# Optimization experiments

Measured on AMD Instinct MI355X. Metric: run time of the kernel, lower is better.

The kernel has to match this reference:

```python
import jax, jax.numpy as jnp
import numpy as np

B, T, D, U = 32, 2048, 512, 512


def setup_inputs() -> dict:
    key = jax.random.key(0)
    ks = jax.random.split(key, 6)
    value = jax.random.normal(ks[0], (B, T, D), dtype=jnp.float32)
    query = jax.random.normal(ks[1], (B, D), dtype=jnp.float32)
    mask = jax.random.randint(ks[2], (B, T), 0, 2, dtype=jnp.int32)
    # Glorot-ish scaled dense weights (no bias, matching Dense(use_bias=False))
    W1 = jax.random.normal(ks[3], (D, U), dtype=jnp.float32) * (1.0 / np.sqrt(D))
    W2 = jax.random.normal(ks[4], (D, U), dtype=jnp.float32) * (1.0 / np.sqrt(D))
    V = jax.random.normal(ks[5], (U,), dtype=jnp.float32) * (1.0 / np.sqrt(U))
    return {"value": value, "query": query, "mask": mask, "W1": W1, "W2": W2, "V": V}


def reference(value, query, mask, W1, W2, V):
    # Additive (Bahdanau) attention scores: u[b,t] = V . tanh(value[b,t] @ W1 + query[b] @ W2)
    w1_key = jnp.einsum('btd,du->btu', value, W1)          # [B, T, U]
    w2_query = jnp.einsum('bd,du->bu', query, W2)          # [B, U]
    u = jnp.einsum('btu,u->bt', jnp.tanh(w1_key + w2_query[:, None, :]), V)  # [B, T]
    # Masking: add -1e20 where mask == 0 (same as keras reference)
    u = u + (1.0 - mask.astype(u.dtype)) * jnp.asarray(-1e20, dtype=u.dtype)
    a = jax.nn.softmax(u, axis=1)                          # [B, T]
    # Pointer extraction: gather value row at argmax of attention weights
    idx = jnp.argmax(a, axis=1)                            # [B]
    context = jnp.take_along_axis(value, idx[:, None, None], axis=1)[:, 0, :]  # [B, D]
    return (context, a)
```

## Files before the change

### kernel.cpp

```cpp
#include <hip/hip_runtime.h>
#include <hip/hip_bf16.h>
#include <hip/hip_fp16.h>
#include <stdint.h>

#define B_ 32
#define T_ 2048
#define D_ 512
#define U_ 512
#define M_ (B_ * T_)

#define BM 64
#define BK 32
#define AP 8
#define MAXC 4

typedef _Float16 half8  __attribute__((ext_vector_type(8)));
typedef _Float16 half4_t __attribute__((ext_vector_type(4)));
typedef float   floatx4 __attribute__((ext_vector_type(4)));

__device__ __forceinline__ float tanh_fast(float x) {
    float ax = fabsf(x);
    float e  = __expf(2.0f * ax);
    float t  = 1.0f - 2.0f / (e + 1.0f);
    return copysignf(t, x);
}

__device__ __forceinline__ void gld_lds16(const void* gsrc, void* lds_dst) {
    typedef __attribute__((address_space(1))) const char gch;
    typedef __attribute__((address_space(3))) char lch;
    __builtin_amdgcn_global_load_lds((const gch*)(uintptr_t)gsrc,
                                     (lch*)(uint32_t)(uintptr_t)lds_dst,
                                     16, 0, 0);
}

__global__ __launch_bounds__(256)
void k_transpose_w1(const float* __restrict__ W1, _Float16* __restrict__ W1T) {
    __shared__ float tile[64][65];
    const int bx = blockIdx.x & 7;
    const int by = blockIdx.x >> 3;
    const int k0 = bx * 64, n0 = by * 64;
    const int tx = threadIdx.x & 63;
    const int ty = threadIdx.x >> 6;
#pragma unroll
    for (int i = 0; i < 16; ++i) {
        int r = ty * 16 + i;
        tile[r][tx] = W1[(size_t)(k0 + r) * U_ + n0 + tx];
    }
    __syncthreads();
#pragma unroll
    for (int i = 0; i < 16; ++i) {
        int r = ty * 16 + i;
        W1T[(size_t)(n0 + r) * D_ + k0 + tx] = (_Float16)tile[tx][r];
    }
}

__global__ __launch_bounds__(256)
void k_w2q(const float* __restrict__ query, const float* __restrict__ W2,
           float* __restrict__ w2q) {
    __shared__ float sq[D_];
    const int b = blockIdx.x;
    const int tid = threadIdx.x;
    sq[tid]       = query[b * D_ + tid];
    sq[tid + 256] = query[b * D_ + tid + 256];
    __syncthreads();
#pragma unroll
    for (int j = 0; j < 2; ++j) {
        const int n = tid + j * 256;
        float acc = 0.f;
#pragma unroll 16
        for (int d = 0; d < D_; ++d)
            acc = fmaf(sq[d], W2[(size_t)d * U_ + n], acc);
        w2q[b * U_ + n] = acc;
    }
}

__global__ __launch_bounds__(512)
void k_gemm_u(const float* __restrict__ value,
              const _Float16* __restrict__ W1T,
              const float* __restrict__ w2q,
              const float* __restrict__ Vv,
              float* __restrict__ u_out) {
    __shared__ __align__(16) _Float16 sA[BM * (BK + AP)];
    __shared__ __align__(16) _Float16 sB[U_ * BK];
    __shared__ float sW2q[U_];
    __shared__ float sV[U_];
    __shared__ float sRed[8][BM];

    const int tid  = threadIdx.x;
    const int wave = tid >> 6;
    const int lane = tid & 63;
    const int l15  = lane & 15;
    const int lg   = lane >> 4;
    const int m0   = blockIdx.x * BM;
    const int b    = m0 >> 11;

    sW2q[tid] = w2q[b * U_ + tid];
    sV[tid]   = Vv[tid];

    floatx4 acc[4][4];
    const floatx4 zero4 = {0.f, 0.f, 0.f, 0.f};
#pragma unroll
    for (int i = 0; i < 4; ++i)
#pragma unroll
        for (int j = 0; j < 4; ++j) acc[i][j] = zero4;

    const int ar = tid >> 3;
    const int ac = (tid & 7) * 4;
    const float* aptr = value + (size_t)(m0 + ar) * D_ + ac;

    const int bn = lane >> 2;
    const int bk = (lane & 3) * 8;

    for (int it = 0; it < 16; ++it) {
        const int k0 = it * BK;
        __syncthreads();
        {
            const floatx4 v4 = *(const floatx4*)(aptr + k0);
            half4_t h;
            h[0] = (_Float16)v4[0]; h[1] = (_Float16)v4[1];
            h[2] = (_Float16)v4[2]; h[3] = (_Float16)v4[3];
            *(half4_t*)(&sA[ar * (BK + AP) + ac]) = h;
        }
#pragma unroll
        for (int jj = 0; jj < 4; ++jj) {
            const int inst = wave * 4 + jj;
            const int n = inst * 16 + bn;
            gld_lds16(W1T + (size_t)n * D_ + k0 + bk, (void*)(sB + inst * 512));
        }
        __syncthreads();

        half8 af[4], bf[4];
#pragma unroll
        for (int mi = 0; mi < 4; ++mi)
            af[mi] = *(const half8*)(&sA[(mi * 16 + l15) * (BK + AP) + lg * 8]);
#pragma unroll
        for (int ni = 0; ni < 4; ++ni) {
            const int n = wave * 64 + ni * 16 + l15;
            bf[ni] = *(const half8*)(&sB[n * BK + lg * 8]);
        }
#pragma unroll
        for (int ni = 0; ni < 4; ++ni)
#pragma unroll
            for (int mi = 0; mi < 4; ++mi)
                acc[mi][ni] = __builtin_amdgcn_mfma_f32_16x16x32_f16(
                    af[mi], bf[ni], acc[mi][ni], 0, 0, 0);
    }

    float ps[4][4];
#pragma unroll
    for (int mi = 0; mi < 4; ++mi)
#pragma unroll
        for (int j = 0; j < 4; ++j) ps[mi][j] = 0.f;

#pragma unroll
    for (int ni = 0; ni < 4; ++ni) {
        const int n = wave * 64 + ni * 16 + l15;
        const float w2 = sW2q[n];
        const float vv = sV[n];
#pragma unroll
        for (int mi = 0; mi < 4; ++mi)
#pragma unroll
            for (int j = 0; j < 4; ++j)
                ps[mi][j] += vv * tanh_fast(acc[mi][ni][j] + w2);
    }
#pragma unroll
    for (int off = 1; off < 16; off <<= 1)
#pragma unroll
        for (int mi = 0; mi < 4; ++mi)
#pragma unroll
            for (int j = 0; j < 4; ++j)
                ps[mi][j] += __shfl_xor(ps[mi][j], off, 64);

    if (l15 == 0) {
#pragma unroll
        for (int mi = 0; mi < 4; ++mi)
#pragma unroll
            for (int j = 0; j < 4; ++j)
                sRed[wave][mi * 16 + lg * 4 + j] = ps[mi][j];
    }
    __syncthreads();
    if (tid < BM) {
        float s = 0.f;
#pragma unroll
        for (int w = 0; w < 8; ++w) s += sRed[w][tid];
        u_out[m0 + tid] = s;
    }
}

__global__ __launch_bounds__(256)
void k_softmax_top(const float* __restrict__ u, const int* __restrict__ mask,
                   float* __restrict__ a_out, int* __restrict__ cand_t) {
    __shared__ float sx[T_];
    __shared__ float rv[4];
    __shared__ int   ri[4];
    __shared__ float s_scalar;

    const int b = blockIdx.x;
    const int tid = threadIdx.x;
    const int wave = tid >> 6, lane = tid & 63;

#pragma unroll
    for (int i = 0; i < 8; ++i) {
        const int t = tid * 8 + i;
        float x = u[b * T_ + t];
        if (mask[b * T_ + t] == 0) x = -1e20f;
        sx[t] = x;
    }
    __syncthreads();

    for (int r = 0; r < MAXC; ++r) {
        float v = -INFINITY; int vi = 0;
#pragma unroll
        for (int i = 0; i < 8; ++i) {
            const int t = tid * 8 + i;
            const float x = sx[t];
            if (x > v) { v = x; vi = t; }
        }
        for (int off = 32; off > 0; off >>= 1) {
            const float ov = __shfl_down(v, off, 64);
            const int   oi = __shfl_down(vi, off, 64);
            if (ov > v || (ov == v && oi < vi)) { v = ov; vi = oi; }
        }
        if (lane == 0) { rv[wave] = v; ri[wave] = vi; }
        __syncthreads();
        if (tid == 0) {
            float bv = rv[0]; int bi = ri[0];
            for (int w = 1; w < 4; ++w)
                if (rv[w] > bv || (rv[w] == bv && ri[w] < bi)) { bv = rv[w]; bi = ri[w]; }
            cand_t[b * MAXC + r] = bi;
            if (r == 0) s_scalar = bv;
            sx[bi] = -INFINITY;
        }
        __syncthreads();
    }
    const float mx = s_scalar;

    float zloc = 0.f;
    float evals[8];
#pragma unroll
    for (int i = 0; i < 8; ++i) {
        const int t = tid * 8 + i;
        float x = u[b * T_ + t];
        if (mask[b * T_ + t] == 0) x = -1e20f;
        const float e = __expf(x - mx);
        evals[i] = e;
        zloc += e;
    }
    for (int off = 32; off > 0; off >>= 1) zloc += __shfl_down(zloc, off, 64);
    if (lane == 0) rv[wave] = zloc;
    __syncthreads();
    if (tid == 0) s_scalar = 1.0f / (rv[0] + rv[1] + rv[2] + rv[3]);
    __syncthreads();
    const float rz = s_scalar;
#pragma unroll
    for (int i = 0; i < 8; ++i) {
        const int t = tid * 8 + i;
        a_out[b * T_ + t] = evals[i] * rz;
    }
}

__global__ __launch_bounds__(256)
void k_rescore(const float* __restrict__ value, const float* __restrict__ W1,
               const float* __restrict__ w2q, const float* __restrict__ Vv,
               const int* __restrict__ mask, const int* __restrict__ cand_t,
               float* __restrict__ cand_score) {
    __shared__ float vrow[D_];
    __shared__ float rsum[4];
    const int b  = blockIdx.x >> 2;
    const int ci = blockIdx.x & 3;
    const int t  = cand_t[b * MAXC + ci];
    const int tid = threadIdx.x;
    const int wave = tid >> 6, lane = tid & 63;
    vrow[tid]       = value[((size_t)b * T_ + t) * D_ + tid];
    vrow[tid + 256] = value[((size_t)b * T_ + t) * D_ + tid + 256];
    __syncthreads();
    float acc = 0.f;
#pragma unroll
    for (int j = 0; j < 2; ++j) {
        const int n = tid + j * 256;
        float dot = 0.f;
#pragma unroll 16
        for (int d = 0; d < D_; ++d)
            dot = fmaf(vrow[d], W1[(size_t)d * U_ + n], dot);
        acc += Vv[n] * tanhf(dot + w2q[b * U_ + n]);
    }
    for (int off = 32; off > 0; off >>= 1) acc += __shfl_down(acc, off, 64);
    if (lane == 0) rsum[wave] = acc;
    __syncthreads();
    if (tid == 0) {
        float s = rsum[0] + rsum[1] + rsum[2] + rsum[3];
        if (mask[b * T_ + t] == 0) s = -1e20f;
        cand_score[b * MAXC + ci] = s;
    }
}

__global__ __launch_bounds__(128)
void k_finalize(const float* __restrict__ value, const int* __restrict__ cand_t,
                const float* __restrict__ cand_score, float* __restrict__ ctx_out) {
    __shared__ int s_t;
    const int b = blockIdx.x;
    const int tid = threadIdx.x;
    if (tid == 0) {
        float bv = cand_score[b * MAXC + 0]; int bt = cand_t[b * MAXC + 0];
        for (int i = 1; i < MAXC; ++i) {
            const float v = cand_score[b * MAXC + i];
            const int   t = cand_t[b * MAXC + i];
            if (v > bv || (v == bv && t < bt)) { bv = v; bt = t; }
        }
        s_t = bt;
    }
    __syncthreads();
    const int t = s_t;
    const floatx4* src = (const floatx4*)(value + ((size_t)b * T_ + t) * D_);
    floatx4* dst = (floatx4*)(ctx_out + b * D_);
    dst[tid] = src[tid];
}

extern "C" void kernel_launch(void* const* d_in, const int* in_sizes, int n_in,
                              void* d_out, int out_size, void* d_ws, size_t ws_size,
                              hipStream_t stream) {
    const float* value = (const float*)d_in[0];
    const float* query = (const float*)d_in[1];
    const int*   mask  = (const int*)d_in[2];
    const float* W1    = (const float*)d_in[3];
    const float* W2    = (const float*)d_in[4];
    const float* Vv    = (const float*)d_in[5];

    char* ws = (char*)d_ws;
    _Float16* W1T   = (_Float16*)ws;
    float*    w2q   = (float*)(ws + 524288);
    float*    u_ws  = (float*)(ws + 524288 + 65536);
    int*      candt = (int*)(ws + 851968);
    float*    cands = (float*)(ws + 852992);

    float* ctx_out = (float*)d_out;
    float* a_out   = (float*)d_out + B_ * D_;

    hipLaunchKernelGGL(k_transpose_w1, dim3(64), dim3(256), 0, stream, W1, W1T);
    hipLaunchKernelGGL(k_w2q,          dim3(32), dim3(256), 0, stream, query, W2, w2q);
    hipLaunchKernelGGL(k_gemm_u,       dim3(M_ / BM), dim3(512), 0, stream,
                       value, W1T, w2q, Vv, u_ws);
    hipLaunchKernelGGL(k_softmax_top,  dim3(32), dim3(256), 0, stream,
                       u_ws, mask, a_out, candt);
    hipLaunchKernelGGL(k_rescore,      dim3(32 * MAXC), dim3(256), 0, stream,
                       value, W1, w2q, Vv, mask, candt, cands);
    hipLaunchKernelGGL(k_finalize,     dim3(32), dim3(128), 0, stream,
                       value, candt, cands, ctx_out);
}
```

Measured before the change: 312.5 us.

## Fuse prep and post kernels, preload A tile, double-buffer W1 in GEMM

Merges the W1 transpose and query projection into one prep launch, with the projection split across more blocks. Merges softmax/top-k, candidate rescoring and context gather into one post kernel, cutting six launches to three. In the GEMM, the whole 64x512 value tile is converted to fp16 and held in LDS once, and W1T K-slices are double-buffered with one barrier per iteration. The larger LDS footprint (about 65KB A plus 64KB B) may lower occupancy, and the post kernel now does the rescoring with only 32 blocks.

```diff
diff --git a/kernel.cpp b/kernel.cpp
--- a/kernel.cpp
+++ b/kernel.cpp
@@ -11,11 +11,10 @@
 
 #define BM 64
 #define BK 32
-#define AP 8
+#define SAW 520
 #define MAXC 4
 
 typedef _Float16 half8  __attribute__((ext_vector_type(8)));
-typedef _Float16 half4_t __attribute__((ext_vector_type(4)));
 typedef float   floatx4 __attribute__((ext_vector_type(4)));
 
 __device__ __forceinline__ float tanh_fast(float x) {
@@ -34,43 +33,48 @@
 }
 
 __global__ __launch_bounds__(256)
-void k_transpose_w1(const float* __restrict__ W1, _Float16* __restrict__ W1T) {
-    __shared__ float tile[64][65];
-    const int bx = blockIdx.x & 7;
-    const int by = blockIdx.x >> 3;
-    const int k0 = bx * 64, n0 = by * 64;
-    const int tx = threadIdx.x & 63;
-    const int ty = threadIdx.x >> 6;
-#pragma unroll
-    for (int i = 0; i < 16; ++i) {
-        int r = ty * 16 + i;
-        tile[r][tx] = W1[(size_t)(k0 + r) * U_ + n0 + tx];
-    }
-    __syncthreads();
-#pragma unroll
-    for (int i = 0; i < 16; ++i) {
-        int r = ty * 16 + i;
-        W1T[(size_t)(n0 + r) * D_ + k0 + tx] = (_Float16)tile[tx][r];
-    }
-}
-
-__global__ __launch_bounds__(256)
-void k_w2q(const float* __restrict__ query, const float* __restrict__ W2,
-           float* __restrict__ w2q) {
-    __shared__ float sq[D_];
-    const int b = blockIdx.x;
+void k_prep(const float* __restrict__ W1, const float* __restrict__ query,
+            const float* __restrict__ W2, _Float16* __restrict__ W1T,
+            float* __restrict__ w2q) {
+    const int bid = blockIdx.x;
     const int tid = threadIdx.x;
-    sq[tid]       = query[b * D_ + tid];
-    sq[tid + 256] = query[b * D_ + tid + 256];
-    __syncthreads();
-#pragma unroll
-    for (int j = 0; j < 2; ++j) {
-        const int n = tid + j * 256;
+    if (bid < 64) {
+        __shared__ float tile[64][65];
+        const int bx = bid & 7;
+        const int by = bid >> 3;
+        const int k0 = bx * 64, n0 = by * 64;
+        const int tx = tid & 63;
+        const int ty = tid >> 6;
+#pragma unroll
+        for (int i = 0; i < 16; ++i) {
+            int r = ty * 16 + i;
+            tile[r][tx] = W1[(size_t)(k0 + r) * U_ + n0 + tx];
+        }
+        __syncthreads();
+#pragma unroll
+        for (int i = 0; i < 16; ++i) {
+            int r = ty * 16 + i;
+            W1T[(size_t)(n0 + r) * D_ + k0 + tx] = (_Float16)tile[tx][r];
+        }
+    } else {
+        __shared__ float sq[D_];
+        __shared__ float part[128];
+        const int id = bid - 64;
+        const int b  = id >> 2;
+        const int nq = id & 3;
+        sq[tid]       = query[b * D_ + tid];
+        sq[tid + 256] = query[b * D_ + tid + 256];
+        __syncthreads();
+        const int n  = nq * 128 + (tid & 127);
+        const int dh = tid >> 7;
         float acc = 0.f;
+        const int d0 = dh * 256;
 #pragma unroll 16
-        for (int d = 0; d < D_; ++d)
+        for (int d = d0; d < d0 + 256; ++d)
             acc = fmaf(sq[d], W2[(size_t)d * U_ + n], acc);
-        w2q[b * U_ + n] = acc;
+        if (dh == 1) part[tid & 127] = acc;
+        __syncthreads();
+        if (dh == 0) w2q[b * U_ + n] = acc + part[tid];
     }
 }
 
@@ -80,8 +84,8 @@
               const float* __restrict__ w2q,
               const float* __restrict__ Vv,
               float* __restrict__ u_out) {
-    __shared__ __align__(16) _Float16 sA[BM * (BK + AP)];
-    __shared__ __align__(16) _Float16 sB[U_ * BK];
+    __shared__ __align__(16) _Float16 sA[BM * SAW];
+    __shared__ __align__(16) _Float16 sB[2][U_ * BK];
     __shared__ float sW2q[U_];
     __shared__ float sV[U_];
     __shared__ float sRed[8][BM];
@@ -97,6 +101,30 @@
     sW2q[tid] = w2q[b * U_ + tid];
     sV[tid]   = Vv[tid];
 
+    const int bn  = lane >> 2;
+    const int bk8 = (lane & 3) * 8;
+
+#pragma unroll
+    for (int jj = 0; jj < 4; ++jj) {
+        const int inst = wave * 4 + jj;
+        const int n = inst * 16 + bn;
+        gld_lds16(W1T + (size_t)n * D_ + bk8, (void*)(&sB[0][inst * 512]));
+    }
+
+#pragma unroll
+    for (int j = 0; j < 8; ++j) {
+        const int row = wave * 8 + j;
+        const float* src = value + (size_t)(m0 + row) * D_ + lane * 8;
+        const floatx4 x0 = *(const floatx4*)(src);
+        const floatx4 x1 = *(const floatx4*)(src + 4);
+        half8 h;
+        h[0] = (_Float16)x0[0]; h[1] = (_Float16)x0[1];
+        h[2] = (_Float16)x0[2]; h[3] = (_Float16)x0[3];
+        h[4] = (_Float16)x1[0]; h[5] = (_Float16)x1[1];
+        h[6] = (_Float16)x1[2]; h[7] = (_Float16)x1[3];
+        *(half8*)(&sA[row * SAW + lane * 8]) = h;
+    }
+
     floatx4 acc[4][4];
     const floatx4 zero4 = {0.f, 0.f, 0.f, 0.f};
 #pragma unroll
@@ -104,39 +132,28 @@
 #pragma unroll
         for (int j = 0; j < 4; ++j) acc[i][j] = zero4;
 
-    const int ar = tid >> 3;
-    const int ac = (tid & 7) * 4;
-    const float* aptr = value + (size_t)(m0 + ar) * D_ + ac;
-
-    const int bn = lane >> 2;
-    const int bk = (lane & 3) * 8;
-
-    for (int it = 0; it < 16; ++it) {
-        const int k0 = it * BK;
-        __syncthreads();
-        {
-            const floatx4 v4 = *(const floatx4*)(aptr + k0);
-            half4_t h;
-            h[0] = (_Float16)v4[0]; h[1] = (_Float16)v4[1];
-            h[2] = (_Float16)v4[2]; h[3] = (_Float16)v4[3];
-            *(half4_t*)(&sA[ar * (BK + AP) + ac]) = h;
-        }
-#pragma unroll
-        for (int jj = 0; jj < 4; ++jj) {
-            const int inst = wave * 4 + jj;
-            const int n = inst * 16 + bn;
-            gld_lds16(W1T + (size_t)n * D_ + k0 + bk, (void*)(sB + inst * 512));
-        }
-        __syncthreads();
-
+    __syncthreads();
+
+    for (int kk = 0; kk < 16; ++kk) {
+        const int cur = kk & 1;
+        if (kk < 15) {
+            const int k0n = (kk + 1) * BK;
+#pragma unroll
+            for (int jj = 0; jj < 4; ++jj) {
+                const int inst = wave * 4 + jj;
+                const int n = inst * 16 + bn;
+                gld_lds16(W1T + (size_t)n * D_ + k0n + bk8,
+                          (void*)(&sB[cur ^ 1][inst * 512]));
+            }
+        }
         half8 af[4], bf[4];
 #pragma unroll
         for (int mi = 0; mi < 4; ++mi)
-            af[mi] = *(const half8*)(&sA[(mi * 16 + l15) * (BK + AP) + lg * 8]);
+            af[mi] = *(const half8*)(&sA[(mi * 16 + l15) * SAW + kk * BK + lg * 8]);
 #pragma unroll
         for (int ni = 0; ni < 4; ++ni) {
             const int n = wave * 64 + ni * 16 + l15;
-            bf[ni] = *(const half8*)(&sB[n * BK + lg * 8]);
+            bf[ni] = *(const half8*)(&sB[cur][n * BK + lg * 8]);
         }
 #pragma unroll
         for (int ni = 0; ni < 4; ++ni)
@@ -144,6 +161,7 @@
             for (int mi = 0; mi < 4; ++mi)
                 acc[mi][ni] = __builtin_amdgcn_mfma_f32_16x16x32_f16(
                     af[mi], bf[ni], acc[mi][ni], 0, 0, 0);
+        __syncthreads();
     }
 
     float ps[4][4];
@@ -188,12 +206,18 @@
 }
 
 __global__ __launch_bounds__(256)
-void k_softmax_top(const float* __restrict__ u, const int* __restrict__ mask,
-                   float* __restrict__ a_out, int* __restrict__ cand_t) {
+void k_post(const float* __restrict__ u, const int* __restrict__ mask,
+            const float* __restrict__ value, const float* __restrict__ W1,
+            const float* __restrict__ w2q, const float* __restrict__ Vv,
+            float* __restrict__ a_out, float* __restrict__ ctx_out) {
     __shared__ float sx[T_];
     __shared__ float rv[4];
     __shared__ int   ri[4];
     __shared__ float s_scalar;
+    __shared__ int   s_cand[MAXC];
+    __shared__ float s_score[MAXC];
+    __shared__ __align__(16) float vrows[MAXC][D_];
+    __shared__ int   s_t;
 
     const int b = blockIdx.x;
     const int tid = threadIdx.x;
@@ -227,7 +251,7 @@
             float bv = rv[0]; int bi = ri[0];
             for (int w = 1; w < 4; ++w)
                 if (rv[w] > bv || (rv[w] == bv && ri[w] < bi)) { bv = rv[w]; bi = ri[w]; }
-            cand_t[b * MAXC + r] = bi;
+            s_cand[r] = bi;
             if (r == 0) s_scalar = bv;
             sx[bi] = -INFINITY;
         }
@@ -257,63 +281,80 @@
         const int t = tid * 8 + i;
         a_out[b * T_ + t] = evals[i] * rz;
     }
-}
-
-__global__ __launch_bounds__(256)
-void k_rescore(const float* __restrict__ value, const float* __restrict__ W1,
-               const float* __restrict__ w2q, const float* __restrict__ Vv,
-               const int* __restrict__ mask, const int* __restrict__ cand_t,
-               float* __restrict__ cand_score) {
-    __shared__ float vrow[D_];
-    __shared__ float rsum[4];
-    const int b  = blockIdx.x >> 2;
-    const int ci = blockIdx.x & 3;
-    const int t  = cand_t[b * MAXC + ci];
-    const int tid = threadIdx.x;
-    const int wave = tid >> 6, lane = tid & 63;
-    vrow[tid]       = value[((size_t)b * T_ + t) * D_ + tid];
-    vrow[tid + 256] = value[((size_t)b * T_ + t) * D_ + tid + 256];
-    __syncthreads();
-    float acc = 0.f;
-#pragma unroll
-    for (int j = 0; j < 2; ++j) {
-        const int n = tid + j * 256;
-        float dot = 0.f;
-#pragma unroll 16
-        for (int d = 0; d < D_; ++d)
-            dot = fmaf(vrow[d], W1[(size_t)d * U_ + n], dot);
-        acc += Vv[n] * tanhf(dot + w2q[b * U_ + n]);
-    }
-    for (int off = 32; off > 0; off >>= 1) acc += __shfl_down(acc, off, 64);
-    if (lane == 0) rsum[wave] = acc;
+
+#pragma unroll
+    for (int ci = 0; ci < MAXC; ++ci) {
+        const int t = s_cand[ci];
+        vrows[ci][tid]       = value[((size_t)b * T_ + t) * D_ + tid];
+        vrows[ci][tid + 256] = value[((size_t)b * T_ + t) * D_ + tid + 256];
+    }
+    __syncthreads();
+
+    float dots[2][MAXC];
+#pragma unroll
+    for (int j = 0; j < 2; ++j)
+#pragma unroll
+        for (int ci = 0; ci < MAXC; ++ci) dots[j][ci] = 0.f;
+
+    for (int d4 = 0; d4 < D_; d4 += 4) {
+        floatx4 vr[MAXC];
+#pragma unroll
+        for (int ci = 0; ci < MAXC; ++ci)
+            vr[ci] = *(const floatx4*)(&vrows[ci][d4]);
+#pragma unroll
+        for (int k = 0; k < 4; ++k) {
+            const float w0 = W1[(size_t)(d4 + k) * U_ + tid];
+            const float w1 = W1[(size_t)(d4 + k) * U_ + tid + 256];
+#pragma unroll
+            for (int ci = 0; ci < MAXC; ++ci) {
+                dots[0][ci] = fmaf(vr[ci][k], w0, dots[0][ci]);
+                dots[1][ci] = fmaf(vr[ci][k], w1, dots[1][ci]);
+            }
+        }
+    }
+    float sc[MAXC];
+#pragma unroll
+    for (int ci = 0; ci < MAXC; ++ci) {
+        const float n0v = Vv[tid]       * tanhf(dots[0][ci] + w2q[b * U_ + tid]);
+        const float n1v = Vv[tid + 256] * tanhf(dots[1][ci] + w2q[b * U_ + tid + 256]);
+        sc[ci] = n0v + n1v;
+    }
+#pragma unroll
+    for (int ci = 0; ci < MAXC; ++ci)
+        for (int off = 32; off > 0; off >>= 1)
+            sc[ci] += __shfl_down(sc[ci], off, 64);
+    if (lane == 0) {
+#pragma unroll
+        for (int ci = 0; ci < MAXC; ++ci) rv[ci * 0 + ci] = 0.f;
+    }
+    __syncthreads();
+    if (lane == 0) {
+#pragma unroll
+        for (int ci = 0; ci < MAXC; ++ci)
+            vrows[ci][wave] = sc[ci];
+    }
     __syncthreads();
     if (tid == 0) {
-        float s = rsum[0] + rsum[1] + rsum[2] + rsum[3];
-        if (mask[b * T_ + t] == 0) s = -1e20f;
-        cand_score[b * MAXC + ci] = s;
-    }
-}
-
-__global__ __launch_bounds__(128)
-void k_finalize(const float* __restrict__ value, const int* __restrict__ cand_t,
-                const float* __restrict__ cand_score, float* __restrict__ ctx_out) {
-    __shared__ int s_t;
-    const int b = blockIdx.x;
-    const int tid = threadIdx.x;
-    if (tid == 0) {
-        float bv = cand_score[b * MAXC + 0]; int bt = cand_t[b * MAXC + 0];
+#pragma unroll
+        for (int ci = 0; ci < MAXC; ++ci) {
+            const int t = s_cand[ci];
+            float s = vrows[ci][0] + vrows[ci][1] + vrows[ci][2] + vrows[ci][3];
+            if (mask[b * T_ + t] == 0) s = -1e20f;
+            s_score[ci] = s;
+        }
+        float bv = s_score[0]; int bt = s_cand[0];
         for (int i = 1; i < MAXC; ++i) {
-            const float v = cand_score[b * MAXC + i];
-            const int   t = cand_t[b * MAXC + i];
-            if (v > bv || (v == bv && t < bt)) { bv = v; bt = t; }
+            if (s_score[i] > bv || (s_score[i] == bv && s_cand[i] < bt)) {
+                bv = s_score[i]; bt = s_cand[i];
+            }
         }
         s_t = bt;
     }
     __syncthreads();
+
     const int t = s_t;
-    const floatx4* src = (const floatx4*)(value + ((size_t)b * T_ + t) * D_);
-    floatx4* dst = (floatx4*)(ctx_out + b * D_);
-    dst[tid] = src[tid];
+    ctx_out[b * D_ + tid]       = value[((size_t)b * T_ + t) * D_ + tid];
+    ctx_out[b * D_ + tid + 256] = value[((size_t)b * T_ + t) * D_ + tid + 256];
 }
 
 extern "C" void kernel_launch(void* const* d_in, const int* in_sizes, int n_in,
@@ -327,23 +368,17 @@
     const float* Vv    = (const float*)d_in[5];
 
     char* ws = (char*)d_ws;
-    _Float16* W1T   = (_Float16*)ws;
-    float*    w2q   = (float*)(ws + 524288);
-    float*    u_ws  = (float*)(ws + 524288 + 65536);
-    int*      candt = (int*)(ws + 851968);
-    float*    cands = (float*)(ws + 852992);
+    _Float16* W1T  = (_Float16*)ws;
+    float*    w2q  = (float*)(ws + 524288);
+    float*    u_ws = (float*)(ws + 524288 + 65536);
 
     float* ctx_out = (float*)d_out;
     float* a_out   = (float*)d_out + B_ * D_;
 
-    hipLaunchKernelGGL(k_transpose_w1, dim3(64), dim3(256), 0, stream, W1, W1T);
-    hipLaunchKernelGGL(k_w2q,          dim3(32), dim3(256), 0, stream, query, W2, w2q);
-    hipLaunchKernelGGL(k_gemm_u,       dim3(M_ / BM), dim3(512), 0, stream,
+    hipLaunchKernelGGL(k_prep,   dim3(192), dim3(256), 0, stream,
+                       W1, query, W2, W1T, w2q);
+    hipLaunchKernelGGL(k_gemm_u, dim3(M_ / BM), dim3(512), 0, stream,
                        value, W1T, w2q, Vv, u_ws);
-    hipLaunchKernelGGL(k_softmax_top,  dim3(32), dim3(256), 0, stream,
-                       u_ws, mask, a_out, candt);
-    hipLaunchKernelGGL(k_rescore,      dim3(32 * MAXC), dim3(256), 0, stream,
-                       value, W1, w2q, Vv, mask, candt, cands);
-    hipLaunchKernelGGL(k_finalize,     dim3(32), dim3(128), 0, stream,
-                       value, candt, cands, ctx_out);
-}
+    hipLaunchKernelGGL(k_post,   dim3(32), dim3(256), 0, stream,
+                       u_ws, mask, value, W1, w2q, Vv, a_out, ctx_out);
+}
```

Measured after the change: 306.9 us. Within noise of the previous version (-1.8%).
